# Performance work log

Hardware: AMD Instinct MI355X
Metric: run time of the kernel (lower is better)

The kernel has to match this reference:

```python
import jax, jax.numpy as jnp
import numpy as np

N_ATOMS = 16384
N_EDGES = 262144
F = 128          # hidden_dim / n_atom_basis
L = 3            # num_interactions
N_RBF = 20
CUTOFF = 5.0
N_MOL = 512
MAX_Z = 100
EPS = 1e-8


def _glorot(k, shape):
    fan_out, fan_in = shape[0], shape[1]
    lim = (6.0 / (fan_in + fan_out)) ** 0.5
    return jax.random.uniform(k, shape, jnp.float32, -lim, lim)


def setup_inputs() -> dict:
    key = jax.random.key(0)
    ks = jax.random.split(key, 8)
    x = jax.random.randint(ks[0], (N_ATOMS,), 1, MAX_Z)            # atomic numbers (0 = padding)
    pos = jax.random.uniform(ks[1], (N_ATOMS, 3), jnp.float32) * 3.0  # box so many d_ij < cutoff
    batch = jnp.sort(jax.random.randint(ks[2], (N_ATOMS,), 0, N_MOL))
    idx_i = jax.random.randint(ks[3], (N_EDGES,), 0, N_ATOMS)
    off = jax.random.randint(ks[4], (N_EDGES,), 1, N_ATOMS)
    idx_j = (idx_i + off) % N_ATOMS                                 # no self loops -> d_ij > 0
    # parameters (torch Linear convention: W is [out, in], y = x @ W.T + b; biases init to 0)
    emb = jax.random.normal(ks[5], (MAX_Z, F), jnp.float32)
    emb = emb.at[0].set(0.0)  # padding_idx=0
    filt_W = _glorot(ks[6], (3 * F, N_RBF))
    filt_b = jnp.zeros((3 * F,), jnp.float32)
    kk = jax.random.split(ks[7], 5 * L)
    inter_W1 = jnp.stack([_glorot(kk[i], (F, F)) for i in range(L)])
    inter_W2 = jnp.stack([_glorot(kk[L + i], (3 * F, F)) for i in range(L)])
    mix_W1 = jnp.stack([_glorot(kk[2 * L + i], (F, 2 * F)) for i in range(L)])
    mix_W2 = jnp.stack([_glorot(kk[3 * L + i], (3 * F, F)) for i in range(L)])
    mix_Wmu = jnp.stack([_glorot(kk[4 * L + i], (2 * F, F)) for i in range(L)])
    inter_b1 = jnp.zeros((L, F), jnp.float32)
    inter_b2 = jnp.zeros((L, 3 * F), jnp.float32)
    mix_b1 = jnp.zeros((L, F), jnp.float32)
    mix_b2 = jnp.zeros((L, 3 * F), jnp.float32)
    return {
        "pos": pos, "emb": emb, "filt_W": filt_W, "filt_b": filt_b,
        "inter_W1": inter_W1, "inter_b1": inter_b1, "inter_W2": inter_W2, "inter_b2": inter_b2,
        "mix_W1": mix_W1, "mix_b1": mix_b1, "mix_W2": mix_W2, "mix_b2": mix_b2, "mix_Wmu": mix_Wmu,
        "x": x, "idx_i": idx_i, "idx_j": idx_j, "batch": batch, "n_mol": N_MOL,
    }


def reference(pos, emb, filt_W, filt_b, inter_W1, inter_b1, inter_W2, inter_b2,
              mix_W1, mix_b1, mix_W2, mix_b2, mix_Wmu,
              x, idx_i, idx_j, batch, n_mol):
    n_atoms = pos.shape[0]
    # edge geometry
    r_ij = pos[idx_j] - pos[idx_i]                          # [E, 3]
    d = jnp.linalg.norm(r_ij, axis=1, keepdims=True)        # [E, 1]
    dir_ij = r_ij / d                                       # [E, 3]
    # Gaussian RBF expansion + cosine cutoff (shared filters)
    offsets = jnp.linspace(0.0, CUTOFF, N_RBF)
    width = offsets[1] - offsets[0]
    phi = jnp.exp((-0.5 / width ** 2) * (d[..., None] - offsets) ** 2)   # [E, 1, R]
    fcut = jnp.where(d < CUTOFF, 0.5 * (jnp.cos(d * jnp.pi / CUTOFF) + 1.0), 0.0)  # [E, 1]
    Wij = (phi @ filt_W.T + filt_b) * fcut[..., None]       # [E, 1, 3F]
    # initial atom features
    q = emb[x][:, None, :]                                  # [N, 1, F]
    mu = jnp.zeros((n_atoms, 3, F), q.dtype)                # [N, 3, F]
    for l in range(L):
        # --- PaiNNInteraction: gather j, filter-mul, split, scatter-add to i ---
        h = jax.nn.silu(q @ inter_W1[l].T + inter_b1[l]) @ inter_W2[l].T + inter_b2[l]  # [N,1,3F]
        xj = Wij * h[idx_j]                                 # [E, 1, 3F]
        dq, dmuR, dmumu = jnp.split(xj, 3, axis=-1)
        q = q + jax.ops.segment_sum(dq, idx_i, num_segments=n_atoms)
        dmu = dmuR * dir_ij[:, :, None] + dmumu * mu[idx_j]  # [E, 3, F]
        mu = mu + jax.ops.segment_sum(dmu, idx_i, num_segments=n_atoms)
        # --- PaiNNMixing ---
        mu_mix = mu @ mix_Wmu[l].T                          # [N, 3, 2F]
        mu_V, mu_W = jnp.split(mu_mix, 2, axis=-1)
        mu_Vn = jnp.sqrt(jnp.sum(mu_V ** 2, axis=-2, keepdims=True) + EPS)  # [N, 1, F]
        ctx = jnp.concatenate([q, mu_Vn], axis=-1)          # [N, 1, 2F]
        g = jax.nn.silu(ctx @ mix_W1[l].T + mix_b1[l]) @ mix_W2[l].T + mix_b2[l]  # [N,1,3F]
        dq_i, dmu_i, dqmu_i = jnp.split(g, 3, axis=-1)
        q = q + dq_i + dqmu_i * jnp.sum(mu_V * mu_W, axis=1, keepdims=True)
        mu = mu + dmu_i * mu_W
    # readout: sum-pool scalar features per molecule
    out = jax.ops.segment_sum(q[:, 0, :], batch, num_segments=n_mol)  # [M, F]
    return out
```

## Files before the change

### kernel.cpp

```cpp
#include <hip/hip_runtime.h>

#define N_ATOMS 16384
#define N_EDGES 262144
#define NRBF 20

static const size_t OFF_T    = 0;
static const size_t OFF_REC  = OFF_T   + (size_t)N_ATOMS*128;
static const size_t OFF_Q    = OFF_REC + (size_t)25*N_EDGES;
static const size_t OFF_H    = OFF_Q   + (size_t)N_ATOMS*128;
static const size_t OFF_MU0  = OFF_H   + (size_t)N_ATOMS*384;
static const size_t OFF_MU1  = OFF_MU0 + (size_t)N_ATOMS*384;
static const size_t OFF_CTX  = OFF_MU1 + (size_t)N_ATOMS*384;
static const size_t OFF_MM   = OFF_CTX + (size_t)N_ATOMS*256;
static const size_t OFF_INT  = OFF_MM  + (size_t)N_ATOMS*768;
static const size_t WS_NEEDED_BYTES = (OFF_INT + (size_t)3*N_ATOMS + 64) * 4;

__global__ __launch_bounds__(256) void hist_kernel(const int* __restrict__ idx_i,
                                                   int* __restrict__ counts) {
  int e = blockIdx.x * 256 + threadIdx.x;
  atomicAdd(&counts[idx_i[e]], 1);
}

__global__ __launch_bounds__(256) void scan_kernel(const int* __restrict__ counts,
                                                   int* __restrict__ row_ptr) {
  __shared__ int part[256];
  int t = threadIdx.x;
  int base = t * 64;
  int s = 0;
  for (int k = 0; k < 64; ++k) s += counts[base + k];
  part[t] = s;
  __syncthreads();
  for (int off = 1; off < 256; off <<= 1) {
    int v = (t >= off) ? part[t - off] : 0;
    __syncthreads();
    part[t] += v;
    __syncthreads();
  }
  int run = (t > 0) ? part[t - 1] : 0;
  for (int k = 0; k < 64; ++k) { row_ptr[base + k] = run; run += counts[base + k]; }
  if (t == 255) row_ptr[N_ATOMS] = run;
}

__global__ __launch_bounds__(256) void scatter_kernel(
    const int* __restrict__ idx_i, const int* __restrict__ row_ptr,
    int* __restrict__ cursor, int* __restrict__ edge_ord) {
  int e = blockIdx.x * 256 + threadIdx.x;
  int i = idx_i[e];
  int p = atomicAdd(&cursor[i], 1);
  edge_ord[row_ptr[i] + p] = e;
}

__global__ __launch_bounds__(256) void prep_kernel(
    const float* __restrict__ pos, const int* __restrict__ idx_i,
    const int* __restrict__ idx_j, const int* __restrict__ edge_ord,
    float* __restrict__ rec) {
  int t = blockIdx.x * 256 + threadIdx.x;
  int e = edge_ord[t];
  int i = idx_i[e], j = idx_j[e];
  float xi = pos[3*i], yi = pos[3*i+1], zi = pos[3*i+2];
  float xj = pos[3*j], yj = pos[3*j+1], zj = pos[3*j+2];
  float dx = xj - xi, dy = yj - yi, dz = zj - zi;
  float d = sqrtf(dx*dx + dy*dy + dz*dz);
  float inv = 1.0f / d;
  float fc = (d < 5.0f) ? 0.5f * (cosf(d * 0.62831853071795864769f) + 1.0f) : 0.0f;
  float* r = rec + (size_t)t * 25;
  r[0] = __int_as_float(j);
  r[1] = dx * inv; r[2] = dy * inv; r[3] = dz * inv; r[4] = fc;
  const float kw = 5.0f / 19.0f;
  const float c2 = (-0.5f / (kw * kw)) * 1.44269504088896340736f;
  #pragma unroll
  for (int k = 0; k < NRBF; ++k) {
    float tt = d - kw * (float)k;
    r[5 + k] = fc * exp2f(c2 * tt * tt);
  }
}

__global__ __launch_bounds__(256) void init_kernel(
    const int* __restrict__ x, const float* __restrict__ emb,
    float* __restrict__ q) {
  int idx = blockIdx.x * 256 + threadIdx.x;
  int a = idx >> 7, f = idx & 127;
  q[idx] = emb[(size_t)x[a]*128 + f];
}

template <int SILU>
__global__ __launch_bounds__(256) void gemm_tn(
    const float* __restrict__ A, const float* __restrict__ B,
    const float* __restrict__ bias, float* __restrict__ C,
    int M, int N, int K) {
  __shared__ float As[32][132];
  __shared__ float Bs[32][68];
  const int tid = threadIdx.x;
  const int m0 = blockIdx.x * 128;
  const int n0 = blockIdx.y * 64;
  const int tx = tid & 15;
  const int ty = tid >> 4;
  const int lrow = tid >> 3;
  const int lk4  = (tid & 7) * 4;
  float acc[8][4] = {};
  for (int k0 = 0; k0 < K; k0 += 32) {
    __syncthreads();
    #pragma unroll
    for (int r = 0; r < 4; ++r) {
      int row = lrow + 32 * r;
      float4 v = *(const float4*)&A[(size_t)(m0 + row) * K + k0 + lk4];
      As[lk4+0][row] = v.x; As[lk4+1][row] = v.y;
      As[lk4+2][row] = v.z; As[lk4+3][row] = v.w;
    }
    #pragma unroll
    for (int r = 0; r < 2; ++r) {
      int row = lrow + 32 * r;
      float4 v = *(const float4*)&B[(size_t)(n0 + row) * K + k0 + lk4];
      Bs[lk4+0][row] = v.x; Bs[lk4+1][row] = v.y;
      Bs[lk4+2][row] = v.z; Bs[lk4+3][row] = v.w;
    }
    __syncthreads();
    #pragma unroll
    for (int kk = 0; kk < 32; ++kk) {
      float4 a0 = *(const float4*)&As[kk][ty*8];
      float4 a1 = *(const float4*)&As[kk][ty*8+4];
      float4 b0 = *(const float4*)&Bs[kk][tx*4];
      float av[8] = {a0.x,a0.y,a0.z,a0.w,a1.x,a1.y,a1.z,a1.w};
      float bv[4] = {b0.x,b0.y,b0.z,b0.w};
      #pragma unroll
      for (int i = 0; i < 8; ++i)
        #pragma unroll
        for (int j = 0; j < 4; ++j)
          acc[i][j] = fmaf(av[i], bv[j], acc[i][j]);
    }
  }
  #pragma unroll
  for (int i = 0; i < 8; ++i) {
    int m = m0 + ty*8 + i;
    float4 o;
    float* po = &o.x;
    #pragma unroll
    for (int j = 0; j < 4; ++j) {
      int n = n0 + tx*4 + j;
      float c = acc[i][j] + (bias ? bias[n] : 0.0f);
      if (SILU) c = c / (1.0f + expf(-c));
      po[j] = c;
    }
    *(float4*)&C[(size_t)m * N + n0 + tx*4] = o;
  }
}

template <int L0>
__global__ __launch_bounds__(256, 4) void edge_kernel(
    const float* __restrict__ rec,
    const float* __restrict__ filtW, const float* __restrict__ filtb,
    const float* __restrict__ h, const float* __restrict__ mu_c,
    const int* __restrict__ row_ptr,
    float* __restrict__ q, float* __restrict__ mu_n) {
  const int lane = threadIdx.x & 63;
  const int half = (threadIdx.x >> 6) & 1;
  const int slot = __builtin_amdgcn_readfirstlane(threadIdx.x >> 7);
  const int a = blockIdx.x * 2 + slot;
  const int f = half * 64 + lane;
  float fw[3][20], fb3[3];
  #pragma unroll
  for (int s = 0; s < 3; ++s) {
    int c = s * 128 + f;
    fb3[s] = filtb[c];
    #pragma unroll
    for (int k = 0; k < 20; ++k) fw[s][k] = filtW[c * 20 + k];
  }
  const int rs = row_ptr[a], re = row_ptr[a + 1];
  float accq = 0.f, am0 = 0.f, am1 = 0.f, am2 = 0.f;
  #pragma unroll 2
  for (int t = rs; t < re; ++t) {
    const float* r = rec + (size_t)t * 25;
    const int j = __float_as_int(r[0]);
    const float dx = r[1], dy = r[2], dz = r[3], fc = r[4];
    const size_t hb = (size_t)j * 384 + f;
    const float hq = h[hb], hr = h[hb + 128], hm = h[hb + 256];
    float mj0 = 0.f, mj1 = 0.f, mj2 = 0.f;
    if (!L0) {
      mj0 = mu_c[hb]; mj1 = mu_c[hb + 128]; mj2 = mu_c[hb + 256];
    }
    float w0 = fc * fb3[0], w1 = fc * fb3[1], w2 = fc * fb3[2];
    #pragma unroll
    for (int k = 0; k < 20; ++k) {
      const float p = r[5 + k];
      w0 = fmaf(p, fw[0][k], w0);
      w1 = fmaf(p, fw[1][k], w1);
      w2 = fmaf(p, fw[2][k], w2);
    }
    accq = fmaf(w0, hq, accq);
    const float xr = w1 * hr;
    const float xm = w2 * hm;
    if (!L0) {
      am0 = fmaf(xr, dx, fmaf(xm, mj0, am0));
      am1 = fmaf(xr, dy, fmaf(xm, mj1, am1));
      am2 = fmaf(xr, dz, fmaf(xm, mj2, am2));
    } else {
      am0 = fmaf(xr, dx, am0);
      am1 = fmaf(xr, dy, am1);
      am2 = fmaf(xr, dz, am2);
    }
  }
  q[(size_t)a * 128 + f] += accq;
  const size_t mb = (size_t)a * 384 + f;
  if (L0) {
    mu_n[mb] = am0; mu_n[mb + 128] = am1; mu_n[mb + 256] = am2;
  } else {
    mu_n[mb]       = mu_c[mb]       + am0;
    mu_n[mb + 128] = mu_c[mb + 128] + am1;
    mu_n[mb + 256] = mu_c[mb + 256] + am2;
  }
}

__global__ __launch_bounds__(256) void ctx_kernel(
    const float* __restrict__ q, const float* __restrict__ mm,
    float* __restrict__ ctx) {
  int idx = blockIdx.x * 256 + threadIdx.x;
  int a = idx >> 7, f = idx & 127;
  size_t b = (size_t)a * 768;
  float v0 = mm[b + f], v1 = mm[b + 256 + f], v2 = mm[b + 512 + f];
  float vn = sqrtf(fmaf(v0, v0, fmaf(v1, v1, v2 * v2)) + 1e-8f);
  ctx[(size_t)a * 256 + f] = q[idx];
  ctx[(size_t)a * 256 + 128 + f] = vn;
}

__global__ __launch_bounds__(256) void mixup_kernel(
    const float* __restrict__ g, const float* __restrict__ mm,
    float* __restrict__ q, float* __restrict__ mu) {
  int idx = blockIdx.x * 256 + threadIdx.x;
  int a = idx >> 7, f = idx & 127;
  size_t b = (size_t)a * 768;
  float v0 = mm[b + f],       v1 = mm[b + 256 + f], v2 = mm[b + 512 + f];
  float w0 = mm[b + 128 + f], w1 = mm[b + 384 + f], w2 = mm[b + 640 + f];
  float svw = fmaf(v0, w0, fmaf(v1, w1, v2 * w2));
  size_t gb = (size_t)a * 384;
  float dq = g[gb + f], dmu = g[gb + 128 + f], dqmu = g[gb + 256 + f];
  q[idx] += dq + dqmu * svw;
  size_t mb = (size_t)a * 384;
  mu[mb + f]       += dmu * w0;
  mu[mb + 128 + f] += dmu * w1;
  mu[mb + 256 + f] += dmu * w2;
}

__global__ __launch_bounds__(128) void readout_kernel(
    const float* __restrict__ q, const int* __restrict__ batch,
    float* __restrict__ out) {
  int m = blockIdx.x;
  int f = threadIdx.x;
  int lo = 0, hi = N_ATOMS;
  while (lo < hi) { int mid = (lo + hi) >> 1; if (batch[mid] < m) lo = mid + 1; else hi = mid; }
  int start = lo;
  hi = N_ATOMS;
  while (lo < hi) { int mid = (lo + hi) >> 1; if (batch[mid] < m + 1) lo = mid + 1; else hi = mid; }
  int end = lo;
  float s = 0.0f;
  for (int a = start; a < end; ++a) s += q[(size_t)a * 128 + f];
  out[(size_t)m * 128 + f] = s;
}

extern "C" void kernel_launch(void* const* d_in, const int* in_sizes, int n_in,
                              void* d_out, int out_size, void* d_ws, size_t ws_size,
                              hipStream_t stream) {
  const float* pos      = (const float*)d_in[0];
  const float* emb      = (const float*)d_in[1];
  const float* filt_W   = (const float*)d_in[2];
  const float* filt_b   = (const float*)d_in[3];
  const float* inter_W1 = (const float*)d_in[4];
  const float* inter_b1 = (const float*)d_in[5];
  const float* inter_W2 = (const float*)d_in[6];
  const float* inter_b2 = (const float*)d_in[7];
  const float* mix_W1   = (const float*)d_in[8];
  const float* mix_b1   = (const float*)d_in[9];
  const float* mix_W2   = (const float*)d_in[10];
  const float* mix_b2   = (const float*)d_in[11];
  const float* mix_Wmu  = (const float*)d_in[12];
  const int*   x        = (const int*)d_in[13];
  const int*   idx_i    = (const int*)d_in[14];
  const int*   idx_j    = (const int*)d_in[15];
  const int*   batch    = (const int*)d_in[16];
  float* out = (float*)d_out;

  if (ws_size < WS_NEEDED_BYTES) return;

  float* wsf    = (float*)d_ws;
  float* t      = wsf + OFF_T;
  float* rec    = wsf + OFF_REC;
  float* q      = wsf + OFF_Q;
  float* h      = wsf + OFF_H;
  float* mu0    = wsf + OFF_MU0;
  float* mu1    = wsf + OFF_MU1;
  float* ctx    = wsf + OFF_CTX;
  float* mm     = wsf + OFF_MM;
  int* wsi      = (int*)(wsf + OFF_INT);
  int* counts   = wsi;
  int* cursor   = wsi + N_ATOMS;
  int* row_ptr  = wsi + 2 * N_ATOMS;
  int* edge_ord = (int*)t;

  hipMemsetAsync(counts, 0, 2 * N_ATOMS * sizeof(int), stream);
  hist_kernel<<<N_EDGES/256, 256, 0, stream>>>(idx_i, counts);
  scan_kernel<<<1, 256, 0, stream>>>(counts, row_ptr);
  scatter_kernel<<<N_EDGES/256, 256, 0, stream>>>(idx_i, row_ptr, cursor, edge_ord);
  prep_kernel<<<N_EDGES/256, 256, 0, stream>>>(pos, idx_i, idx_j, edge_ord, rec);
  init_kernel<<<N_ATOMS*128/256, 256, 0, stream>>>(x, emb, q);

  float* mu_c = mu0;
  float* mu_n = mu1;
  for (int l = 0; l < 3; ++l) {
    gemm_tn<1><<<dim3(128, 2), 256, 0, stream>>>(
        q, inter_W1 + (size_t)l*128*128, inter_b1 + (size_t)l*128, t, 16384, 128, 128);
    gemm_tn<0><<<dim3(128, 6), 256, 0, stream>>>(
        t, inter_W2 + (size_t)l*384*128, inter_b2 + (size_t)l*384, h, 16384, 384, 128);
    if (l == 0)
      edge_kernel<1><<<N_ATOMS/2, 256, 0, stream>>>(
          rec, filt_W, filt_b, h, mu_c, row_ptr, q, mu_n);
    else
      edge_kernel<0><<<N_ATOMS/2, 256, 0, stream>>>(
          rec, filt_W, filt_b, h, mu_c, row_ptr, q, mu_n);
    gemm_tn<0><<<dim3(384, 4), 256, 0, stream>>>(
        mu_n, mix_Wmu + (size_t)l*256*128, nullptr, mm, 49152, 256, 128);
    ctx_kernel<<<N_ATOMS*128/256, 256, 0, stream>>>(q, mm, ctx);
    gemm_tn<1><<<dim3(128, 2), 256, 0, stream>>>(
        ctx, mix_W1 + (size_t)l*128*256, mix_b1 + (size_t)l*128, t, 16384, 128, 256);
    gemm_tn<0><<<dim3(128, 6), 256, 0, stream>>>(
        t, mix_W2 + (size_t)l*384*128, mix_b2 + (size_t)l*384, h, 16384, 384, 128);
    mixup_kernel<<<N_ATOMS*128/256, 256, 0, stream>>>(h, mm, q, mu_n);
    float* tmp = mu_c; mu_c = mu_n; mu_n = tmp;
  }
  readout_kernel<<<512, 128, 0, stream>>>(q, batch, out);
}
```

Measured before the change: 965.3 us.

## Replace FP32 SIMT GEMM with split-bf16 MFMA GEMM (3-term hi/lo)

Rewrites the dense node-level GEMM kernel to use bf16 matrix-core MFMA instructions. Each fp32 operand is split into high and low bf16 parts, and three products (hh, hl, lh) are accumulated in fp32 to approximate fp32 accuracy. The goal is to move the GEMM FLOPs from scalar FMA to matrix cores. In exchange it adds per-element conversion work when staging tiles into shared memory, and the output stores become scalar and less coalesced than the old float4 writes.

```diff
diff --git a/kernel.cpp b/kernel.cpp
--- a/kernel.cpp
+++ b/kernel.cpp
@@ -3,6 +3,10 @@
 #define N_ATOMS 16384
 #define N_EDGES 262144
 #define NRBF 20
+
+typedef __bf16 bf16x8 __attribute__((ext_vector_type(8)));
+typedef __bf16 bf16x4 __attribute__((ext_vector_type(4)));
+typedef float f32x4 __attribute__((ext_vector_type(4)));
 
 static const size_t OFF_T    = 0;
 static const size_t OFF_REC  = OFF_T   + (size_t)N_ATOMS*128;
@@ -84,65 +88,95 @@
 }
 
 template <int SILU>
-__global__ __launch_bounds__(256) void gemm_tn(
+__global__ __launch_bounds__(256) void gemm_mfma(
     const float* __restrict__ A, const float* __restrict__ B,
     const float* __restrict__ bias, float* __restrict__ C,
     int M, int N, int K) {
-  __shared__ float As[32][132];
-  __shared__ float Bs[32][68];
-  const int tid = threadIdx.x;
+  __shared__ __bf16 Ah[128][40];
+  __shared__ __bf16 Al[128][40];
+  __shared__ __bf16 Bh[64][40];
+  __shared__ __bf16 Bl[64][40];
+  const int tid  = threadIdx.x;
+  const int lane = tid & 63;
+  const int w    = tid >> 6;
+  const int wm   = (w >> 1) * 64;
+  const int wn   = (w & 1) * 32;
   const int m0 = blockIdx.x * 128;
   const int n0 = blockIdx.y * 64;
-  const int tx = tid & 15;
-  const int ty = tid >> 4;
-  const int lrow = tid >> 3;
-  const int lk4  = (tid & 7) * 4;
-  float acc[8][4] = {};
+  const int srow = tid >> 3;
+  const int skc  = (tid & 7) * 4;
+  f32x4 acc[4][2] = {};
   for (int k0 = 0; k0 < K; k0 += 32) {
     __syncthreads();
     #pragma unroll
-    for (int r = 0; r < 4; ++r) {
-      int row = lrow + 32 * r;
-      float4 v = *(const float4*)&A[(size_t)(m0 + row) * K + k0 + lk4];
-      As[lk4+0][row] = v.x; As[lk4+1][row] = v.y;
-      As[lk4+2][row] = v.z; As[lk4+3][row] = v.w;
-    }
-    #pragma unroll
-    for (int r = 0; r < 2; ++r) {
-      int row = lrow + 32 * r;
-      float4 v = *(const float4*)&B[(size_t)(n0 + row) * K + k0 + lk4];
-      Bs[lk4+0][row] = v.x; Bs[lk4+1][row] = v.y;
-      Bs[lk4+2][row] = v.z; Bs[lk4+3][row] = v.w;
+    for (int it = 0; it < 4; ++it) {
+      int row = srow + 32 * it;
+      float4 v = *(const float4*)&A[(size_t)(m0 + row) * K + k0 + skc];
+      bf16x4 hv, lv;
+      float vv[4] = {v.x, v.y, v.z, v.w};
+      #pragma unroll
+      for (int jj = 0; jj < 4; ++jj) {
+        __bf16 hb = (__bf16)vv[jj];
+        hv[jj] = hb;
+        lv[jj] = (__bf16)(vv[jj] - (float)hb);
+      }
+      *(bf16x4*)&Ah[row][skc] = hv;
+      *(bf16x4*)&Al[row][skc] = lv;
+    }
+    #pragma unroll
+    for (int it = 0; it < 2; ++it) {
+      int row = srow + 32 * it;
+      float4 v = *(const float4*)&B[(size_t)(n0 + row) * K + k0 + skc];
+      bf16x4 hv, lv;
+      float vv[4] = {v.x, v.y, v.z, v.w};
+      #pragma unroll
+      for (int jj = 0; jj < 4; ++jj) {
+        __bf16 hb = (__bf16)vv[jj];
+        hv[jj] = hb;
+        lv[jj] = (__bf16)(vv[jj] - (float)hb);
+      }
+      *(bf16x4*)&Bh[row][skc] = hv;
+      *(bf16x4*)&Bl[row][skc] = lv;
     }
     __syncthreads();
-    #pragma unroll
-    for (int kk = 0; kk < 32; ++kk) {
-      float4 a0 = *(const float4*)&As[kk][ty*8];
-      float4 a1 = *(const float4*)&As[kk][ty*8+4];
-      float4 b0 = *(const float4*)&Bs[kk][tx*4];
-      float av[8] = {a0.x,a0.y,a0.z,a0.w,a1.x,a1.y,a1.z,a1.w};
-      float bv[4] = {b0.x,b0.y,b0.z,b0.w};
+    const int fr = lane & 15;
+    const int fk = (lane >> 4) * 8;
+    bf16x8 ah[4], al[4], bh[2], bl[2];
+    #pragma unroll
+    for (int mi = 0; mi < 4; ++mi) {
+      ah[mi] = *(const bf16x8*)&Ah[wm + mi*16 + fr][fk];
+      al[mi] = *(const bf16x8*)&Al[wm + mi*16 + fr][fk];
+    }
+    #pragma unroll
+    for (int ni = 0; ni < 2; ++ni) {
+      bh[ni] = *(const bf16x8*)&Bh[wn + ni*16 + fr][fk];
+      bl[ni] = *(const bf16x8*)&Bl[wn + ni*16 + fr][fk];
+    }
+    #pragma unroll
+    for (int mi = 0; mi < 4; ++mi)
       #pragma unroll
-      for (int i = 0; i < 8; ++i)
-        #pragma unroll
-        for (int j = 0; j < 4; ++j)
-          acc[i][j] = fmaf(av[i], bv[j], acc[i][j]);
-    }
-  }
+      for (int ni = 0; ni < 2; ++ni) {
+        acc[mi][ni] = __builtin_amdgcn_mfma_f32_16x16x32_bf16(ah[mi], bh[ni], acc[mi][ni], 0, 0, 0);
+        acc[mi][ni] = __builtin_amdgcn_mfma_f32_16x16x32_bf16(ah[mi], bl[ni], acc[mi][ni], 0, 0, 0);
+        acc[mi][ni] = __builtin_amdgcn_mfma_f32_16x16x32_bf16(al[mi], bh[ni], acc[mi][ni], 0, 0, 0);
+      }
+  }
+  const int cn = lane & 15;
+  const int cr = (lane >> 4) * 4;
   #pragma unroll
-  for (int i = 0; i < 8; ++i) {
-    int m = m0 + ty*8 + i;
-    float4 o;
-    float* po = &o.x;
-    #pragma unroll
-    for (int j = 0; j < 4; ++j) {
-      int n = n0 + tx*4 + j;
-      float c = acc[i][j] + (bias ? bias[n] : 0.0f);
-      if (SILU) c = c / (1.0f + expf(-c));
-      po[j] = c;
-    }
-    *(float4*)&C[(size_t)m * N + n0 + tx*4] = o;
-  }
+  for (int mi = 0; mi < 4; ++mi)
+    #pragma unroll
+    for (int ni = 0; ni < 2; ++ni) {
+      int n = n0 + wn + ni*16 + cn;
+      float bb = bias ? bias[n] : 0.0f;
+      #pragma unroll
+      for (int r = 0; r < 4; ++r) {
+        int m = m0 + wm + mi*16 + cr + r;
+        float c = acc[mi][ni][r] + bb;
+        if (SILU) c = c / (1.0f + expf(-c));
+        C[(size_t)m * N + n] = c;
+      }
+    }
 }
 
 template <int L0>
@@ -305,9 +339,9 @@
   float* mu_c = mu0;
   float* mu_n = mu1;
   for (int l = 0; l < 3; ++l) {
-    gemm_tn<1><<<dim3(128, 2), 256, 0, stream>>>(
+    gemm_mfma<1><<<dim3(128, 2), 256, 0, stream>>>(
         q, inter_W1 + (size_t)l*128*128, inter_b1 + (size_t)l*128, t, 16384, 128, 128);
-    gemm_tn<0><<<dim3(128, 6), 256, 0, stream>>>(
+    gemm_mfma<0><<<dim3(128, 6), 256, 0, stream>>>(
         t, inter_W2 + (size_t)l*384*128, inter_b2 + (size_t)l*384, h, 16384, 384, 128);
     if (l == 0)
       edge_kernel<1><<<N_ATOMS/2, 256, 0, stream>>>(
@@ -315,12 +349,12 @@
     else
       edge_kernel<0><<<N_ATOMS/2, 256, 0, stream>>>(
           rec, filt_W, filt_b, h, mu_c, row_ptr, q, mu_n);
-    gemm_tn<0><<<dim3(384, 4), 256, 0, stream>>>(
+    gemm_mfma<0><<<dim3(384, 4), 256, 0, stream>>>(
         mu_n, mix_Wmu + (size_t)l*256*128, nullptr, mm, 49152, 256, 128);
     ctx_kernel<<<N_ATOMS*128/256, 256, 0, stream>>>(q, mm, ctx);
-    gemm_tn<1><<<dim3(128, 2), 256, 0, stream>>>(
+    gemm_mfma<1><<<dim3(128, 2), 256, 0, stream>>>(
         ctx, mix_W1 + (size_t)l*128*256, mix_b1 + (size_t)l*128, t, 16384, 128, 256);
-    gemm_tn<0><<<dim3(128, 6), 256, 0, stream>>>(
+    gemm_mfma<0><<<dim3(128, 6), 256, 0, stream>>>(
         t, mix_W2 + (size_t)l*384*128, mix_b2 + (size_t)l*384, h, 16384, 384, 128);
     mixup_kernel<<<N_ATOMS*128/256, 256, 0, stream>>>(h, mm, q, mu_n);
     float* tmp = mu_c; mu_c = mu_n; mu_n = tmp;
```

After: 773.9 us. 19.8% less time.
